# Kernel tuning notes

Measured on AMD Instinct MI355X. Metric: run time of the kernel, lower is better.

Reference implementation:

```python
import jax, jax.numpy as jnp
import numpy as np

C = 16      # num_mixture_elements (classes)
DIM = 16    # dim_latent
L = 6       # radial_layers (flow_length)
N = 200000  # number of latent samples


def setup_inputs() -> dict:
    key = jax.random.key(0)
    k_z, k_z0, k_la, k_b = jax.random.split(key, 4)
    z = jax.random.normal(k_z, (N, DIM), dtype=jnp.float32)
    # Radial flow parameters, one set per flow layer, batched over classes c
    z0 = jax.random.normal(k_z0, (L, C, DIM), dtype=jnp.float32) * 0.1
    log_alpha = jax.random.normal(k_la, (L, C), dtype=jnp.float32) * 0.1
    beta = jax.random.normal(k_b, (L, C), dtype=jnp.float32) * 0.1
    # Base Gaussian parameters (zeros / identity, non-trainable buffers in torch)
    mean = jnp.zeros((C, DIM), dtype=jnp.float32)
    cov = jnp.broadcast_to(jnp.eye(DIM, dtype=jnp.float32), (C, DIM, DIM)).copy()
    return {"z": z, "z0": z0, "log_alpha": log_alpha, "beta": beta,
            "mean": mean, "cov": cov}


def _flow_step(carry, params):
    """One batched Radial transform: z -> z + beta * h(alpha, r) * (z - z0)."""
    z, slj = carry                 # z: [c, N, dim], slj: [c, N]
    z0_l, la_l, b_l = params       # [c, dim], [c], [c]
    dim = z.shape[-1]
    z_sub = z - z0_l[:, None, :]                        # [c, N, dim]
    r = jnp.linalg.norm(z_sub, axis=-1, keepdims=True)  # [c, N, 1]
    alpha = jnp.exp(la_l)[:, None, None]                # [c, 1, 1]
    beta = b_l[:, None, None]                           # [c, 1, 1]
    h = 1.0 / (alpha + r)
    z_next = z + beta * h * z_sub
    bh = beta * h
    # log|det J| = (d-1)*log(1 + beta*h) + log(1 + beta*h + beta*h'(r)*r), h' = -h^2
    log_det = (dim - 1) * jnp.log1p(bh) + jnp.log1p(bh - beta * r * h * h)
    return (z_next, slj + log_det[..., 0]), None


def reference(z, z0, log_alpha, beta, mean, cov):
    c, dim = mean.shape
    zc = jnp.broadcast_to(z[None], (c,) + z.shape)       # z.repeat(c,1,1) -> [c,N,dim]
    slj0 = jnp.zeros(zc.shape[:2], dtype=z.dtype)        # [c, N]
    (zk, slj), _ = jax.lax.scan(_flow_step, (zc, slj0), (z0, log_alpha, beta))
    # MultivariateNormal(mean, cov) log_prob, batched over classes c
    L_chol = jnp.linalg.cholesky(cov)                    # [c, dim, dim]
    diff = zk - mean[:, None, :]                         # [c, N, dim]
    sol = jax.vmap(lambda Lc, d: jax.scipy.linalg.solve_triangular(Lc, d.T, lower=True).T)(L_chol, diff)
    log2pi = jnp.float32(np.log(2.0 * np.pi))
    half_logdet = jnp.sum(jnp.log(jnp.diagonal(L_chol, axis1=-2, axis2=-1)), axis=-1)  # [c]
    log_prob_z = -0.5 * (dim * log2pi + jnp.sum(sol * sol, axis=-1)) - half_logdet[:, None]
    log_q_c = (log_prob_z + slj).T                       # transpose(0,1) -> [N, c]
    # eval-mode NaN masking: log_q_c[isnan] = -inf
    return jnp.where(jnp.isnan(log_q_c), -jnp.inf, log_q_c)
```

## Files before the change

### kernel.cpp

```cpp
#include <hip/hip_runtime.h>
#include <math.h>

#define NC 16
#define DIM 16
#define LAYERS 6

typedef float v2f __attribute__((ext_vector_type(2)));

#define WS_LINV  0
#define WS_MU2   4096
#define WS_CST   4352
#define WS_ALPHA 4368
#define WS_TOT   4464

__global__ void __launch_bounds__(64) prep_kernel(
    const float* __restrict__ cov, const float* __restrict__ log_alpha,
    const float* __restrict__ mean, float* __restrict__ ws) {
    __shared__ float A[DIM * 17];
    __shared__ float B[DIM * DIM];
    const int c = blockIdx.x;
    const int t = threadIdx.x;
    for (int k = t; k < DIM * DIM; k += 64) {
        int r = k >> 4, j = k & 15;
        A[r * 17 + j] = cov[c * 256 + k];
    }
    __syncthreads();
    const int i = t & 15;
    const bool act = t < 16;
    for (int k = 0; k < DIM; ++k) {
        if (act && i == k) A[k * 17 + k] = sqrtf(A[k * 17 + k]);
        __syncthreads();
        if (act && i > k) A[i * 17 + k] /= A[k * 17 + k];
        __syncthreads();
        if (act && i > k) {
            float lik = A[i * 17 + k];
            for (int j2 = k + 1; j2 <= i; ++j2)
                A[i * 17 + j2] -= lik * A[j2 * 17 + k];
        }
        __syncthreads();
    }
    const int j = i;
    float x[DIM];
    #pragma unroll
    for (int r = 0; r < DIM; ++r) {
        float s = (r == j) ? 1.0f : 0.0f;
        #pragma unroll
        for (int k = 0; k < r; ++k) s = fmaf(-A[r * 17 + k], x[k], s);
        x[r] = s / A[r * 17 + r];
    }
    if (act) {
        #pragma unroll
        for (int r = 0; r < DIM; ++r) {
            B[r * 16 + j] = x[r];
            ws[WS_LINV + c * 256 + r * 16 + j] = x[r];
        }
    }
    __syncthreads();
    if (t == 0) {
        float hld = 0.0f;
        #pragma unroll
        for (int r = 0; r < DIM; ++r) hld += __logf(A[r * 17 + r]);
        const float log2pi = 1.8378770664093453f;
        ws[WS_CST + c] = -0.5f * (float)DIM * log2pi - hld;
    }
    if (t < LAYERS) ws[WS_ALPHA + t * NC + c] = __expf(log_alpha[t * NC + c]);
    if (act) {
        float m2 = 0.0f;
        #pragma unroll
        for (int jj = 0; jj < DIM; ++jj)
            m2 = fmaf(B[i * 16 + jj], mean[c * DIM + jj], m2);
        ws[WS_MU2 + c * 16 + i] = m2;
    }
}

__global__ void __launch_bounds__(256) density_kernel(
    const float* __restrict__ z, const float* __restrict__ z0,
    const float* __restrict__ beta, const float* __restrict__ ws,
    float* __restrict__ out, int N) {
    __shared__ float tile[64 * 5];
    const int tid = threadIdx.x;
    const int lane = tid & 63;
    const int wv = tid >> 6;
    const int c = __builtin_amdgcn_readfirstlane(blockIdx.y * 4 + wv);
    const int s = blockIdx.x * 64 + lane;
    const int sl = s < N ? s : N - 1;

    v2f zc2[8];
    {
        const float4* zp = (const float4*)(z + (size_t)sl * DIM);
        float4 a0 = zp[0], a1 = zp[1], a2 = zp[2], a3 = zp[3];
        zc2[0] = (v2f){a0.x, a0.y}; zc2[1] = (v2f){a0.z, a0.w};
        zc2[2] = (v2f){a1.x, a1.y}; zc2[3] = (v2f){a1.z, a1.w};
        zc2[4] = (v2f){a2.x, a2.y}; zc2[5] = (v2f){a2.z, a2.w};
        zc2[6] = (v2f){a3.x, a3.y}; zc2[7] = (v2f){a3.z, a3.w};
    }

    float slj2 = 0.0f;
    #pragma unroll
    for (int l = 0; l < LAYERS; ++l) {
        const v2f* z0p = (const v2f*)(z0 + (l * NC + c) * DIM);
        v2f d2[8];
        v2f r2a = (v2f){0.0f, 0.0f}, r2b = (v2f){0.0f, 0.0f};
        #pragma unroll
        for (int k = 0; k < 8; ++k) {
            d2[k] = zc2[k] - z0p[k];
            if (k & 1) r2b = __builtin_elementwise_fma(d2[k], d2[k], r2b);
            else       r2a = __builtin_elementwise_fma(d2[k], d2[k], r2a);
        }
        v2f r2v = r2a + r2b;
        float r = __builtin_amdgcn_sqrtf(r2v.x + r2v.y);
        float al = ws[WS_ALPHA + l * NC + c];
        float b  = beta[l * NC + c];
        float h  = __builtin_amdgcn_rcpf(al + r);
        float bh = b * h;
        v2f bh2 = (v2f){bh, bh};
        #pragma unroll
        for (int k = 0; k < 8; ++k)
            zc2[k] = __builtin_elementwise_fma(bh2, d2[k], zc2[k]);
        float t2 = fmaf(-(b * r * h), h, bh);
        float lg = __builtin_amdgcn_logf(1.0f + bh);
        float lt = __builtin_amdgcn_logf(1.0f + t2);
        slj2 = fmaf(15.0f, lg, slj2) + lt;
    }

    const v2f* Li2 = (const v2f*)(ws + WS_LINV + c * 256);
    const float* m2 = ws + WS_MU2 + c * 16;
    float q = 0.0f;
    #pragma unroll
    for (int i = 0; i < DIM; ++i) {
        v2f acc2 = (v2f){0.0f, 0.0f};
        #pragma unroll
        for (int jj = 0; jj <= (i >> 1); ++jj)
            acc2 = __builtin_elementwise_fma(Li2[i * 8 + jj], zc2[jj], acc2);
        float acc = (acc2.x + acc2.y) - m2[i];
        q = fmaf(acc, acc, q);
    }

    const float ln2 = 0.6931471805599453f;
    float res = ws[WS_CST + c] + fmaf(-0.5f, q, slj2 * ln2);
    if (res != res) res = -INFINITY;

    tile[lane * 5 + wv] = res;
    __syncthreads();
    const int srow = tid >> 2, col = tid & 3;
    const int gs = blockIdx.x * 64 + srow;
    if (gs < N) out[(size_t)gs * NC + blockIdx.y * 4 + col] = tile[srow * 5 + col];
}

extern "C" void kernel_launch(void* const* d_in, const int* in_sizes, int n_in,
                              void* d_out, int out_size, void* d_ws, size_t ws_size,
                              hipStream_t stream) {
    const float* z    = (const float*)d_in[0];
    const float* z0   = (const float*)d_in[1];
    const float* la   = (const float*)d_in[2];
    const float* beta = (const float*)d_in[3];
    const float* mean = (const float*)d_in[4];
    const float* cov  = (const float*)d_in[5];
    float* out = (float*)d_out;
    float* ws  = (float*)d_ws;
    const int N = in_sizes[0] / DIM;

    hipLaunchKernelGGL(prep_kernel, dim3(NC), dim3(64), 0, stream, cov, la, mean, ws);
    const int nb = (N + 63) / 64;
    hipLaunchKernelGGL(density_kernel, dim3(nb, 4), dim3(256), 0, stream,
                       z, z0, beta, ws, out, N);
}
```

Before: 123.2 us.

## Track z minus z0 across flow layers and interleave class groups in 1D grid

The flow is rewritten to carry d = z - z0_l instead of z. Each layer updates it as d_next = (1+bh)*d + (z0_l - z0_{l+1}), using differences precomputed in the prep kernel. This removes a per-layer subtraction, and the mean subtraction folds into the last layer's offset, dropping the mu2 term from the quadratic form. The grid also becomes 1D with the four class groups of a sample block adjacent, which should improve cache reuse of z. The float rounding changes slightly from the reference formulation.

Measured after the change: 116.1 us. 1.06x faster.

```diff
diff --git a/kernel.cpp b/kernel.cpp
--- a/kernel.cpp
+++ b/kernel.cpp
@@ -8,16 +8,16 @@
 typedef float v2f __attribute__((ext_vector_type(2)));
 
 #define WS_LINV  0
-#define WS_MU2   4096
-#define WS_CST   4352
-#define WS_ALPHA 4368
-#define WS_TOT   4464
+#define WS_CST   4096
+#define WS_ALPHA 4112
+#define WS_DZ0   4208
+#define WS_TOT   5744
 
 __global__ void __launch_bounds__(64) prep_kernel(
     const float* __restrict__ cov, const float* __restrict__ log_alpha,
-    const float* __restrict__ mean, float* __restrict__ ws) {
+    const float* __restrict__ z0, const float* __restrict__ mean,
+    float* __restrict__ ws) {
     __shared__ float A[DIM * 17];
-    __shared__ float B[DIM * DIM];
     const int c = blockIdx.x;
     const int t = threadIdx.x;
     for (int k = t; k < DIM * DIM; k += 64) {
@@ -50,12 +50,9 @@
     }
     if (act) {
         #pragma unroll
-        for (int r = 0; r < DIM; ++r) {
-            B[r * 16 + j] = x[r];
+        for (int r = 0; r < DIM; ++r)
             ws[WS_LINV + c * 256 + r * 16 + j] = x[r];
-        }
     }
-    __syncthreads();
     if (t == 0) {
         float hld = 0.0f;
         #pragma unroll
@@ -65,11 +62,13 @@
     }
     if (t < LAYERS) ws[WS_ALPHA + t * NC + c] = __expf(log_alpha[t * NC + c]);
     if (act) {
-        float m2 = 0.0f;
         #pragma unroll
-        for (int jj = 0; jj < DIM; ++jj)
-            m2 = fmaf(B[i * 16 + jj], mean[c * DIM + jj], m2);
-        ws[WS_MU2 + c * 16 + i] = m2;
+        for (int l = 0; l < LAYERS; ++l) {
+            float cur = z0[(l * NC + c) * DIM + i];
+            float nxt = (l < LAYERS - 1) ? z0[((l + 1) * NC + c) * DIM + i]
+                                         : mean[c * DIM + i];
+            ws[WS_DZ0 + (l * NC + c) * DIM + i] = cur - nxt;
+        }
     }
 }
 
@@ -81,29 +80,29 @@
     const int tid = threadIdx.x;
     const int lane = tid & 63;
     const int wv = tid >> 6;
-    const int c = __builtin_amdgcn_readfirstlane(blockIdx.y * 4 + wv);
-    const int s = blockIdx.x * 64 + lane;
+    const int xb = blockIdx.x >> 2;
+    const int cg = blockIdx.x & 3;
+    const int c = __builtin_amdgcn_readfirstlane(cg * 4 + wv);
+    const int s = xb * 64 + lane;
     const int sl = s < N ? s : N - 1;
 
-    v2f zc2[8];
+    v2f d2[8];
     {
         const float4* zp = (const float4*)(z + (size_t)sl * DIM);
+        const v2f* z0p = (const v2f*)(z0 + c * DIM);
         float4 a0 = zp[0], a1 = zp[1], a2 = zp[2], a3 = zp[3];
-        zc2[0] = (v2f){a0.x, a0.y}; zc2[1] = (v2f){a0.z, a0.w};
-        zc2[2] = (v2f){a1.x, a1.y}; zc2[3] = (v2f){a1.z, a1.w};
-        zc2[4] = (v2f){a2.x, a2.y}; zc2[5] = (v2f){a2.z, a2.w};
-        zc2[6] = (v2f){a3.x, a3.y}; zc2[7] = (v2f){a3.z, a3.w};
+        d2[0] = (v2f){a0.x, a0.y} - z0p[0]; d2[1] = (v2f){a0.z, a0.w} - z0p[1];
+        d2[2] = (v2f){a1.x, a1.y} - z0p[2]; d2[3] = (v2f){a1.z, a1.w} - z0p[3];
+        d2[4] = (v2f){a2.x, a2.y} - z0p[4]; d2[5] = (v2f){a2.z, a2.w} - z0p[5];
+        d2[6] = (v2f){a3.x, a3.y} - z0p[6]; d2[7] = (v2f){a3.z, a3.w} - z0p[7];
     }
 
     float slj2 = 0.0f;
     #pragma unroll
     for (int l = 0; l < LAYERS; ++l) {
-        const v2f* z0p = (const v2f*)(z0 + (l * NC + c) * DIM);
-        v2f d2[8];
-        v2f r2a = (v2f){0.0f, 0.0f}, r2b = (v2f){0.0f, 0.0f};
+        v2f r2a = (v2f){0.f, 0.f}, r2b = (v2f){0.f, 0.f};
         #pragma unroll
         for (int k = 0; k < 8; ++k) {
-            d2[k] = zc2[k] - z0p[k];
             if (k & 1) r2b = __builtin_elementwise_fma(d2[k], d2[k], r2b);
             else       r2a = __builtin_elementwise_fma(d2[k], d2[k], r2a);
         }
@@ -113,26 +112,27 @@
         float b  = beta[l * NC + c];
         float h  = __builtin_amdgcn_rcpf(al + r);
         float bh = b * h;
-        v2f bh2 = (v2f){bh, bh};
+        float g  = 1.0f + bh;
+        float t2 = fmaf(-(b * r * h), h, bh);
+        float lg = __builtin_amdgcn_logf(g);
+        float lt = __builtin_amdgcn_logf(1.0f + t2);
+        slj2 = fmaf(15.0f, lg, slj2) + lt;
+        const v2f* dz = (const v2f*)(ws + WS_DZ0 + (l * NC + c) * DIM);
+        v2f g2 = (v2f){g, g};
         #pragma unroll
         for (int k = 0; k < 8; ++k)
-            zc2[k] = __builtin_elementwise_fma(bh2, d2[k], zc2[k]);
-        float t2 = fmaf(-(b * r * h), h, bh);
-        float lg = __builtin_amdgcn_logf(1.0f + bh);
-        float lt = __builtin_amdgcn_logf(1.0f + t2);
-        slj2 = fmaf(15.0f, lg, slj2) + lt;
+            d2[k] = __builtin_elementwise_fma(g2, d2[k], dz[k]);
     }
 
     const v2f* Li2 = (const v2f*)(ws + WS_LINV + c * 256);
-    const float* m2 = ws + WS_MU2 + c * 16;
     float q = 0.0f;
     #pragma unroll
     for (int i = 0; i < DIM; ++i) {
-        v2f acc2 = (v2f){0.0f, 0.0f};
+        v2f acc2 = (v2f){0.f, 0.f};
         #pragma unroll
         for (int jj = 0; jj <= (i >> 1); ++jj)
-            acc2 = __builtin_elementwise_fma(Li2[i * 8 + jj], zc2[jj], acc2);
-        float acc = (acc2.x + acc2.y) - m2[i];
+            acc2 = __builtin_elementwise_fma(Li2[i * 8 + jj], d2[jj], acc2);
+        float acc = acc2.x + acc2.y;
         q = fmaf(acc, acc, q);
     }
 
@@ -143,8 +143,8 @@
     tile[lane * 5 + wv] = res;
     __syncthreads();
     const int srow = tid >> 2, col = tid & 3;
-    const int gs = blockIdx.x * 64 + srow;
-    if (gs < N) out[(size_t)gs * NC + blockIdx.y * 4 + col] = tile[srow * 5 + col];
+    const int gs = xb * 64 + srow;
+    if (gs < N) out[(size_t)gs * NC + cg * 4 + col] = tile[srow * 5 + col];
 }
 
 extern "C" void kernel_launch(void* const* d_in, const int* in_sizes, int n_in,
@@ -160,8 +160,8 @@
     float* ws  = (float*)d_ws;
     const int N = in_sizes[0] / DIM;
 
-    hipLaunchKernelGGL(prep_kernel, dim3(NC), dim3(64), 0, stream, cov, la, mean, ws);
+    hipLaunchKernelGGL(prep_kernel, dim3(NC), dim3(64), 0, stream, cov, la, z0, mean, ws);
     const int nb = (N + 63) / 64;
-    hipLaunchKernelGGL(density_kernel, dim3(nb, 4), dim3(256), 0, stream,
+    hipLaunchKernelGGL(density_kernel, dim3(nb * 4), dim3(256), 0, stream,
                        z, z0, beta, ws, out, N);
 }
```
